# Optimization experiments

Measured on AMD Instinct MI355X. Metric: run time of the kernel, lower is better.

## Reference

```python
import jax, jax.numpy as jnp
import numpy as np

N_NODES = 50000
N_EDGES = 1_600_000
IN_DIM = 256
OUT_DIM = 128
NEG_SLOPE = 0.01  # F.leaky_relu default


def setup_inputs() -> dict:
    key = jax.random.key(0)
    k1, k2, k3, k4, k5 = jax.random.split(key, 5)
    x = jax.random.normal(k1, (N_NODES, IN_DIM), dtype=jnp.float32)
    # glorot_init: uniform in [-r, r], r = sqrt(6/(in+out))
    r = np.sqrt(6.0 / (IN_DIM + OUT_DIM)).astype(np.float32)
    weight = jax.random.uniform(k2, (IN_DIM, OUT_DIM), dtype=jnp.float32, minval=-r, maxval=r)
    adj_rows = jax.random.randint(k3, (N_EDGES,), 0, N_NODES, dtype=jnp.int64 if jax.config.jax_enable_x64 else jnp.int32)
    adj_cols = jax.random.randint(k4, (N_EDGES,), 0, N_NODES, dtype=jnp.int64 if jax.config.jax_enable_x64 else jnp.int32)
    adj_vals = jax.random.uniform(k5, (N_EDGES,), dtype=jnp.float32)
    return {"x": x, "weight": weight, "adj_vals": adj_vals,
            "adj_rows": adj_rows, "adj_cols": adj_cols}


def reference(x, weight, adj_vals, adj_rows, adj_cols):
    # h = X @ W : [N, OUT_DIM]
    h = x @ weight
    # sparse adj @ h via edge-list SpMM: out[r] += v * h[c]
    msgs = adj_vals[:, None] * h[adj_cols]            # [E, OUT_DIM]
    agg = jax.ops.segment_sum(msgs, adj_rows, num_segments=N_NODES)
    # leaky_relu epilogue
    return jnp.where(agg >= 0, agg, NEG_SLOPE * agg)
```

## Files before the change

### kernel.cpp

```cpp
#include <hip/hip_runtime.h>
#include <hip/hip_fp16.h>

#define N_NODES 50000
#define N_EDGES 1600000
#define IN_DIM 256
#define OUT_DIM 128
#define NEG_SLOPE 0.01f

#define BIN_SH    7
#define BIN_ROWS  128
#define NBIN      ((N_NODES + BIN_ROWS - 1) / BIN_ROWS)
#define CAPB      4864
#define ROWOFF_N  (NBIN * BIN_ROWS + 1)

#define GBLK_ROWS 32
#define NGBLK     ((N_NODES + GBLK_ROWS - 1) / GBLK_ROWS)

#define HIST_BLOCKS 512
#define CONVW_BLOCKS 16
#define EPB_H (N_EDGES / HIST_BLOCKS)
#define SCAT_BLOCKS 512
#define EPB_S (N_EDGES / SCAT_BLOCKS)
#define SCAT_ITERS ((EPB_S + 511) / 512)

typedef _Float16 f16x8 __attribute__((ext_vector_type(8)));
typedef float    f32x4 __attribute__((ext_vector_type(4)));
typedef float    f32x8 __attribute__((ext_vector_type(8)));

__device__ __forceinline__ float lrelu(float v) {
    return v >= 0.f ? v : NEG_SLOPE * v;
}

#define BM 128
#define GEMM_BLOCKS ((N_NODES + BM - 1) / BM)

#define CVT16(lo, hi) do { \
    lo[0]=(_Float16)xr[0].x; lo[1]=(_Float16)xr[0].y; lo[2]=(_Float16)xr[0].z; lo[3]=(_Float16)xr[0].w; \
    lo[4]=(_Float16)xr[1].x; lo[5]=(_Float16)xr[1].y; lo[6]=(_Float16)xr[1].z; lo[7]=(_Float16)xr[1].w; \
    hi[0]=(_Float16)xr[2].x; hi[1]=(_Float16)xr[2].y; hi[2]=(_Float16)xr[2].z; hi[3]=(_Float16)xr[2].w; \
    hi[4]=(_Float16)xr[3].x; hi[5]=(_Float16)xr[3].y; hi[6]=(_Float16)xr[3].z; hi[7]=(_Float16)xr[3].w; \
} while (0)

__global__ __launch_bounds__(256, 2) void gemm_xw_mfma(const float* __restrict__ x,
                                                       const __half* __restrict__ wtl,
                                                       __half* __restrict__ h) {
    __shared__ f16x8 wt8[32 * 128];
    __shared__ f16x8 xs8[2][4][BM];

    const int t    = threadIdx.x;
    const int lane = t & 63;
    const int wv   = t >> 6;
    const int row0 = blockIdx.x * BM;

    {
        const int4* src = (const int4*)wtl;
        int4* dst = (int4*)wt8;
#pragma unroll
        for (int i = 0; i < 16; ++i) dst[i * 256 + t] = src[i * 256 + t];
    }

    const int srow = t >> 1;
    const int skh  = t & 1;
    const int grow = row0 + srow;
    const bool rv  = grow < N_NODES;
    const float* xp = x + (size_t)(rv ? grow : 0) * IN_DIM + skh * 16;

    float4 xr[4];
#pragma unroll
    for (int i = 0; i < 4; ++i)
        xr[i] = rv ? ((const float4*)xp)[i] : make_float4(0.f, 0.f, 0.f, 0.f);
    {
        f16x8 lo, hi;
        CVT16(lo, hi);
        xs8[0][skh * 2 + 0][srow] = lo;
        xs8[0][skh * 2 + 1][srow] = hi;
    }
    __syncthreads();

    f32x4 acc[2][8];
#pragma unroll
    for (int mf = 0; mf < 2; ++mf)
#pragma unroll
        for (int nf = 0; nf < 8; ++nf) acc[mf][nf] = (f32x4){0.f, 0.f, 0.f, 0.f};

    const int kg  = lane >> 4;
    const int l15 = lane & 15;
    const int mb  = (wv << 5) + l15;

#pragma unroll
    for (int ks = 0; ks < 8; ++ks) {
        const int cur = ks & 1;
        if (ks < 7) {
#pragma unroll
            for (int i = 0; i < 4; ++i)
                xr[i] = rv ? ((const float4*)(xp + (ks + 1) * 32))[i]
                           : make_float4(0.f, 0.f, 0.f, 0.f);
        }
        const f16x8 b0 = xs8[cur][kg][mb];
        const f16x8 b1 = xs8[cur][kg][mb + 16];
#pragma unroll
        for (int nf = 0; nf < 8; ++nf) {
            const f16x8 a = wt8[(((ks << 2) | kg) << 7) + (nf << 4) + l15];
            acc[0][nf] = __builtin_amdgcn_mfma_f32_16x16x32_f16(a, b0, acc[0][nf], 0, 0, 0);
            acc[1][nf] = __builtin_amdgcn_mfma_f32_16x16x32_f16(a, b1, acc[1][nf], 0, 0, 0);
        }
        if (ks < 7) {
            f16x8 lo, hi;
            CVT16(lo, hi);
            xs8[cur ^ 1][skh * 2 + 0][srow] = lo;
            xs8[cur ^ 1][skh * 2 + 1][srow] = hi;
            __syncthreads();
        }
    }

    const int rg = lane >> 4;
#pragma unroll
    for (int mf = 0; mf < 2; ++mf) {
        const int m = row0 + (wv << 5) + (mf << 4) + l15;
        if (m < N_NODES) {
            __half* hp = h + (size_t)m * OUT_DIM + (rg << 2);
#pragma unroll
            for (int nf = 0; nf < 8; ++nf) {
                union { ushort4 u; __half f[4]; } o;
                o.f[0] = __float2half(acc[mf][nf][0]);
                o.f[1] = __float2half(acc[mf][nf][1]);
                o.f[2] = __float2half(acc[mf][nf][2]);
                o.f[3] = __float2half(acc[mf][nf][3]);
                *(ushort4*)(hp + (nf << 4)) = o.u;
            }
        }
    }
}

__global__ __launch_bounds__(256) void bucket_hist(const int* __restrict__ rows,
                                                   int* __restrict__ counts,
                                                   const float* __restrict__ w,
                                                   __half* __restrict__ wtl) {
    if (blockIdx.x >= HIST_BLOCKS) {
        const int e0 = ((blockIdx.x - HIST_BLOCKS) * 256 + threadIdx.x) * 8;
        const int k  = e0 >> 7;
        const int n0 = e0 & 127;
        const float4 a = *(const float4*)(w + e0);
        const float4 b = *(const float4*)(w + e0 + 4);
        __half* dst = wtl + ((size_t)((k >> 3) * 128 + n0)) * 8 + (k & 7);
        dst[0]  = __float2half(a.x);
        dst[8]  = __float2half(a.y);
        dst[16] = __float2half(a.z);
        dst[24] = __float2half(a.w);
        dst[32] = __float2half(b.x);
        dst[40] = __float2half(b.y);
        dst[48] = __float2half(b.z);
        dst[56] = __float2half(b.w);
        return;
    }

    __shared__ int lhist[NBIN];
    const int t = threadIdx.x;
    const int ebase = blockIdx.x * EPB_H;

    for (int b = t; b < NBIN; b += 256) lhist[b] = 0;
    __syncthreads();

    for (int k = 0; k < EPB_H; k += 256) {
        if (k + t < EPB_H) atomicAdd(&lhist[rows[ebase + k + t] >> BIN_SH], 1);
    }
    __syncthreads();

    for (int b = t; b < NBIN; b += 256) {
        const int c = lhist[b];
        if (c > 0) atomicAdd(&counts[b], c);
    }
}

__global__ __launch_bounds__(512) void scatter_bins(const int* __restrict__ rows,
                                                    const int* __restrict__ cols,
                                                    const float* __restrict__ vals,
                                                    const int* __restrict__ counts,
                                                    int* __restrict__ cursor,
                                                    int2* __restrict__ ebuf) {
    __shared__ int sb[512];
    __shared__ int lbase[NBIN];
    const int t = threadIdx.x;
    const int ebase = blockIdx.x * EPB_S;

    sb[t] = (t < NBIN) ? counts[t] : 0;
    const int myc = sb[t];
    __syncthreads();
    for (int off = 1; off < 512; off <<= 1) {
        const int u = (t >= off) ? sb[t - off] : 0;
        __syncthreads();
        sb[t] += u;
        __syncthreads();
    }
    if (t < NBIN) lbase[t] = sb[t] - myc;
    __syncthreads();
    if (t < NBIN) sb[t] = 0;
    __syncthreads();

    int myr[SCAT_ITERS];
#pragma unroll
    for (int k = 0; k < SCAT_ITERS; ++k) {
        const int i = k * 512 + t;
        myr[k] = -1;
        if (i < EPB_S) {
            const int r = rows[ebase + i];
            myr[k] = r;
            atomicAdd(&sb[r >> BIN_SH], 1);
        }
    }
    __syncthreads();

    if (t < NBIN) {
        const int c = sb[t];
        sb[t] = (c > 0) ? (lbase[t] + atomicAdd(&cursor[t], c)) : 0;
    }
    __syncthreads();

#pragma unroll
    for (int k = 0; k < SCAT_ITERS; ++k) {
        const int i = k * 512 + t;
        if (i < EPB_S) {
            const int e = ebase + i;
            const int r = myr[k];
            const int pos = atomicAdd(&sb[r >> BIN_SH], 1);
            ebuf[pos] = make_int2(cols[e] | ((r & (BIN_ROWS - 1)) << 16), __float_as_int(vals[e]));
        }
    }
}

__global__ __launch_bounds__(512) void sort_bins(const int* __restrict__ counts,
                                                 int2* __restrict__ ebuf,
                                                 int* __restrict__ rowoff,
                                                 int* __restrict__ ovf) {
    __shared__ int2 srec[CAPB];
    __shared__ int sb[512];
    __shared__ int hist[BIN_ROWS];
    __shared__ int pfx[BIN_ROWS];
    __shared__ int s_base, s_cnt;

    const int t   = threadIdx.x;
    const int bin = blockIdx.x;

    sb[t] = (t < NBIN) ? counts[t] : 0;
    const int myc = sb[t];
    __syncthreads();
    for (int off = 1; off < 512; off <<= 1) {
        const int u = (t >= off) ? sb[t - off] : 0;
        __syncthreads();
        sb[t] += u;
        __syncthreads();
    }
    if (t == bin) { s_base = sb[t] - myc; s_cnt = myc; }
    if (t < BIN_ROWS) hist[t] = 0;
    __syncthreads();
    const int base = s_base;
    const int cnt  = s_cnt;

    if (cnt <= CAPB) {
        for (int i = t; i < cnt; i += 512) {
            const int2 r = ebuf[base + i];
            srec[i] = r;
            atomicAdd(&hist[(r.x >> 16) & (BIN_ROWS - 1)], 1);
        }
        __syncthreads();

        if (t < BIN_ROWS) pfx[t] = hist[t];
        __syncthreads();
        for (int off = 1; off < BIN_ROWS; off <<= 1) {
            const int u = (t >= off && t < BIN_ROWS) ? pfx[t - off] : 0;
            __syncthreads();
            if (t < BIN_ROWS) pfx[t] += u;
            __syncthreads();
        }
        if (t < BIN_ROWS) {
            const int excl = pfx[t] - hist[t];
            rowoff[(bin << BIN_SH) + t] = base + excl;
            if (t == BIN_ROWS - 1) rowoff[(bin << BIN_SH) + BIN_ROWS] = base + cnt;
            hist[t] = excl;
        }
        __syncthreads();

        for (int i = t; i < cnt; i += 512) {
            const int2 r = srec[i];
            const int pos = base + atomicAdd(&hist[(r.x >> 16) & (BIN_ROWS - 1)], 1);
            ebuf[pos] = r;
        }
    } else {
        if (t == 0) ovf[bin] = 1;
        for (int i = t; i < cnt; i += 512)
            atomicAdd(&hist[(ebuf[base + i].x >> 16) & (BIN_ROWS - 1)], 1);
        __syncthreads();
        if (t < BIN_ROWS) pfx[t] = hist[t];
        __syncthreads();
        for (int off = 1; off < BIN_ROWS; off <<= 1) {
            const int u = (t >= off && t < BIN_ROWS) ? pfx[t - off] : 0;
            __syncthreads();
            if (t < BIN_ROWS) pfx[t] += u;
            __syncthreads();
        }
        if (t < BIN_ROWS) {
            rowoff[(bin << BIN_SH) + t] = base + (pfx[t] - hist[t]);
            if (t == BIN_ROWS - 1) rowoff[(bin << BIN_SH) + BIN_ROWS] = base + cnt;
        }
    }
}

__global__ __launch_bounds__(256) void gather_rows(const __half* __restrict__ h,
                                                   const int* __restrict__ rowoff,
                                                   const int2* __restrict__ ebuf,
                                                   const int* __restrict__ ovf,
                                                   float* __restrict__ out) {
    const int t    = threadIdx.x;
    const int w    = t >> 6;
    const int lane = t & 63;
    const int grp  = lane >> 4;
    const int gl   = lane & 15;
    const int bkt  = blockIdx.x;
    const int bin  = bkt >> 2;
    const int rbase = bkt * GBLK_ROWS + w * 8;

    if (ovf[bin]) {
        const int bb = rowoff[bin << BIN_SH];
        const int be = rowoff[(bin << BIN_SH) + BIN_ROWS];
        for (int rr = 0; rr < 8; ++rr) {
            const int row = rbase + rr;
            float2 acc = make_float2(0.f, 0.f);
            for (int e = bb; e < be; ++e) {
                const int2 rec = ebuf[e];
                if (((rec.x >> 16) & (BIN_ROWS - 1)) == (row & (BIN_ROWS - 1))) {
                    const float2 m = __half22float2(((const __half2*)(h + (size_t)(rec.x & 0xFFFF) * OUT_DIM))[lane]);
                    const float v = __int_as_float(rec.y);
                    acc.x += v * m.x; acc.y += v * m.y;
                }
            }
            if (row < N_NODES) {
                acc.x = lrelu(acc.x); acc.y = lrelu(acc.y);
                ((float2*)(out + (size_t)row * OUT_DIM))[lane] = acc;
            }
        }
        return;
    }

    for (int p = 0; p < 4; ++p) {
        const int r0 = rbase + 2 * p;
        const int r1 = r0 + 1;
        const int b0 = rowoff[r0], e0 = rowoff[r0 + 1];
        const int b1 = rowoff[r1], e1 = rowoff[r1 + 1];
        const int n0 = e0 - b0, n1 = e1 - b1;
        const int nmax = n0 > n1 ? n0 : n1;
        const int iters = (nmax + 3) >> 2;

        f32x8 a0 = (f32x8){0.f,0.f,0.f,0.f,0.f,0.f,0.f,0.f};
        f32x8 a1 = (f32x8){0.f,0.f,0.f,0.f,0.f,0.f,0.f,0.f};

        for (int it = 0; it < iters; ++it) {
            const int i0 = b0 + (it << 2) + grp;
            const int i1 = b1 + (it << 2) + grp;
            const bool v0i = i0 < e0;
            const bool v1i = i1 < e1;
            const int2 rA = ebuf[v0i ? i0 : 0];
            const int2 rB = ebuf[v1i ? i1 : 0];
            const float vA = v0i ? __int_as_float(rA.y) : 0.f;
            const float vB = v1i ? __int_as_float(rB.y) : 0.f;
            const f16x8 hA = *(const f16x8*)(h + (size_t)(rA.x & 0xFFFF) * OUT_DIM + (gl << 3));
            const f16x8 hB = *(const f16x8*)(h + (size_t)(rB.x & 0xFFFF) * OUT_DIM + (gl << 3));
#pragma unroll
            for (int j = 0; j < 8; ++j) {
                a0[j] += vA * (float)hA[j];
                a1[j] += vB * (float)hB[j];
            }
        }

#pragma unroll
        for (int j = 0; j < 8; ++j) {
            float x0 = a0[j], x1 = a1[j];
            x0 += __shfl_xor(x0, 16); x0 += __shfl_xor(x0, 32);
            x1 += __shfl_xor(x1, 16); x1 += __shfl_xor(x1, 32);
            a0[j] = x0; a1[j] = x1;
        }

        const int row = (grp & 2) ? r1 : r0;
        float q[4];
#pragma unroll
        for (int k = 0; k < 4; ++k) {
            const float lo = (grp & 2) ? a1[k]     : a0[k];
            const float hi = (grp & 2) ? a1[k + 4] : a0[k + 4];
            q[k] = lrelu((grp & 1) ? hi : lo);
        }
        if (row < N_NODES) {
            float4 o = make_float4(q[0], q[1], q[2], q[3]);
            *(float4*)(out + (size_t)row * OUT_DIM + (gl << 3) + ((grp & 1) << 2)) = o;
        }
    }
}

extern "C" void kernel_launch(void* const* d_in, const int* in_sizes, int n_in,
                              void* d_out, int out_size, void* d_ws, size_t ws_size,
                              hipStream_t stream) {
    const float* x    = (const float*)d_in[0];
    const float* w    = (const float*)d_in[1];
    const float* vals = (const float*)d_in[2];
    const int*   rows = (const int*)d_in[3];
    const int*   cols = (const int*)d_in[4];
    float* out = (float*)d_out;

    char* ws = (char*)d_ws;
    size_t off = 0;
    auto alloc = [&](size_t bytes) {
        void* p = ws + off;
        off = (off + bytes + 255) & ~(size_t)255;
        return p;
    };
    __half* h      = (__half*)alloc((size_t)N_NODES * OUT_DIM * sizeof(__half));
    int2*  ebuf    = (int2*) alloc((size_t)N_EDGES * sizeof(int2));
    __half* wtl    = (__half*)alloc((size_t)IN_DIM * OUT_DIM * sizeof(__half));
    int*   rowoff  = (int*)  alloc((size_t)ROWOFF_N * sizeof(int));
    int*   meta    = (int*)  alloc((size_t)(3 * NBIN) * sizeof(int));
    int*   counts  = meta;
    int*   cursor  = meta + NBIN;
    int*   ovfl    = meta + 2 * NBIN;

    hipMemsetAsync(meta, 0, (size_t)(3 * NBIN) * sizeof(int), stream);

    bucket_hist<<<HIST_BLOCKS + CONVW_BLOCKS, 256, 0, stream>>>(rows, counts, w, wtl);
    gemm_xw_mfma<<<GEMM_BLOCKS, 256, 0, stream>>>(x, wtl, h);
    scatter_bins<<<SCAT_BLOCKS, 512, 0, stream>>>(rows, cols, vals, counts, cursor, ebuf);
    sort_bins<<<NBIN, 512, 0, stream>>>(counts, ebuf, rowoff, ovfl);
    gather_rows<<<NGBLK, 256, 0, stream>>>(h, rowoff, ebuf, ovfl, out);
}
```

Baseline: 238.6 us.

## Fuse per-bin sort with row gather, keeping sorted edges in LDS

Merges the sort_bins and gather_rows kernels into a single sort_gather kernel. Each block sorts its bin's edges straight into shared memory and then runs the SpMM gather for its 128 rows using LDS row offsets. This removes the write-back of sorted edges to global memory, the rowoff and overflow arrays, and one kernel launch. In exchange the gather now runs with only 391 blocks of 512 threads and heavy LDS use, so fewer rows are in flight per CU during the latency-bound h gathers.

```diff
diff --git a/kernel.cpp b/kernel.cpp
--- a/kernel.cpp
+++ b/kernel.cpp
@@ -11,10 +11,6 @@
 #define BIN_ROWS  128
 #define NBIN      ((N_NODES + BIN_ROWS - 1) / BIN_ROWS)
 #define CAPB      4864
-#define ROWOFF_N  (NBIN * BIN_ROWS + 1)
-
-#define GBLK_ROWS 32
-#define NGBLK     ((N_NODES + GBLK_ROWS - 1) / GBLK_ROWS)
 
 #define HIST_BLOCKS 512
 #define CONVW_BLOCKS 16
@@ -228,18 +224,19 @@
     }
 }
 
-__global__ __launch_bounds__(512) void sort_bins(const int* __restrict__ counts,
-                                                 int2* __restrict__ ebuf,
-                                                 int* __restrict__ rowoff,
-                                                 int* __restrict__ ovf) {
+__global__ __launch_bounds__(512) void sort_gather(const int* __restrict__ counts,
+                                                   const int2* __restrict__ ebuf,
+                                                   const __half* __restrict__ h,
+                                                   float* __restrict__ out) {
     __shared__ int2 srec[CAPB];
-    __shared__ int sb[512];
-    __shared__ int hist[BIN_ROWS];
-    __shared__ int pfx[BIN_ROWS];
-    __shared__ int s_base, s_cnt;
+    __shared__ int  hist[BIN_ROWS];
+    __shared__ int  pfx[BIN_ROWS];
+    __shared__ int  rowoff_l[BIN_ROWS + 1];
+    __shared__ int  s_base, s_cnt;
 
     const int t   = threadIdx.x;
     const int bin = blockIdx.x;
+    int* sb = (int*)srec;
 
     sb[t] = (t < NBIN) ? counts[t] : 0;
     const int myc = sb[t];
@@ -256,12 +253,12 @@
     const int base = s_base;
     const int cnt  = s_cnt;
 
+    const int wv   = t >> 6;
+    const int lane = t & 63;
+
     if (cnt <= CAPB) {
-        for (int i = t; i < cnt; i += 512) {
-            const int2 r = ebuf[base + i];
-            srec[i] = r;
-            atomicAdd(&hist[(r.x >> 16) & (BIN_ROWS - 1)], 1);
-        }
+        for (int i = t; i < cnt; i += 512)
+            atomicAdd(&hist[(ebuf[base + i].x >> 16) & (BIN_ROWS - 1)], 1);
         __syncthreads();
 
         if (t < BIN_ROWS) pfx[t] = hist[t];
@@ -274,122 +271,90 @@
         }
         if (t < BIN_ROWS) {
             const int excl = pfx[t] - hist[t];
-            rowoff[(bin << BIN_SH) + t] = base + excl;
-            if (t == BIN_ROWS - 1) rowoff[(bin << BIN_SH) + BIN_ROWS] = base + cnt;
+            rowoff_l[t] = excl;
+            if (t == BIN_ROWS - 1) rowoff_l[BIN_ROWS] = cnt;
             hist[t] = excl;
         }
         __syncthreads();
 
         for (int i = t; i < cnt; i += 512) {
-            const int2 r = srec[i];
-            const int pos = base + atomicAdd(&hist[(r.x >> 16) & (BIN_ROWS - 1)], 1);
-            ebuf[pos] = r;
+            const int2 r = ebuf[base + i];
+            const int pos = atomicAdd(&hist[(r.x >> 16) & (BIN_ROWS - 1)], 1);
+            srec[pos] = r;
+        }
+        __syncthreads();
+
+        const int grp = lane >> 4;
+        const int gl  = lane & 15;
+        for (int rp = 0; rp < 8; ++rp) {
+            const int lr0 = (wv << 4) + 2 * rp;
+            const int lr1 = lr0 + 1;
+            const int b0 = rowoff_l[lr0], e0 = rowoff_l[lr0 + 1];
+            const int b1 = rowoff_l[lr1], e1 = rowoff_l[lr1 + 1];
+            const int n0 = e0 - b0, n1 = e1 - b1;
+            const int nmax = n0 > n1 ? n0 : n1;
+            const int iters = (nmax + 3) >> 2;
+
+            f32x8 a0 = (f32x8){0.f,0.f,0.f,0.f,0.f,0.f,0.f,0.f};
+            f32x8 a1 = (f32x8){0.f,0.f,0.f,0.f,0.f,0.f,0.f,0.f};
+
+            for (int it = 0; it < iters; ++it) {
+                const int i0 = b0 + (it << 2) + grp;
+                const int i1 = b1 + (it << 2) + grp;
+                const bool v0i = i0 < e0;
+                const bool v1i = i1 < e1;
+                const int2 rA = srec[v0i ? i0 : 0];
+                const int2 rB = srec[v1i ? i1 : 0];
+                const float vA = v0i ? __int_as_float(rA.y) : 0.f;
+                const float vB = v1i ? __int_as_float(rB.y) : 0.f;
+                const f16x8 hA = *(const f16x8*)(h + (size_t)(rA.x & 0xFFFF) * OUT_DIM + (gl << 3));
+                const f16x8 hB = *(const f16x8*)(h + (size_t)(rB.x & 0xFFFF) * OUT_DIM + (gl << 3));
+#pragma unroll
+                for (int j = 0; j < 8; ++j) {
+                    a0[j] += vA * (float)hA[j];
+                    a1[j] += vB * (float)hB[j];
+                }
+            }
+
+#pragma unroll
+            for (int j = 0; j < 8; ++j) {
+                float x0 = a0[j], x1 = a1[j];
+                x0 += __shfl_xor(x0, 16); x0 += __shfl_xor(x0, 32);
+                x1 += __shfl_xor(x1, 16); x1 += __shfl_xor(x1, 32);
+                a0[j] = x0; a1[j] = x1;
+            }
+
+            const int lrow = (grp & 2) ? lr1 : lr0;
+            const int grow = (bin << BIN_SH) + lrow;
+            float q[4];
+#pragma unroll
+            for (int k = 0; k < 4; ++k) {
+                const float lo = (grp & 2) ? a1[k]     : a0[k];
+                const float hi = (grp & 2) ? a1[k + 4] : a0[k + 4];
+                q[k] = lrelu((grp & 1) ? hi : lo);
+            }
+            if (grow < N_NODES) {
+                float4 o = make_float4(q[0], q[1], q[2], q[3]);
+                *(float4*)(out + (size_t)grow * OUT_DIM + (gl << 3) + ((grp & 1) << 2)) = o;
+            }
         }
     } else {
-        if (t == 0) ovf[bin] = 1;
-        for (int i = t; i < cnt; i += 512)
-            atomicAdd(&hist[(ebuf[base + i].x >> 16) & (BIN_ROWS - 1)], 1);
-        __syncthreads();
-        if (t < BIN_ROWS) pfx[t] = hist[t];
-        __syncthreads();
-        for (int off = 1; off < BIN_ROWS; off <<= 1) {
-            const int u = (t >= off && t < BIN_ROWS) ? pfx[t - off] : 0;
-            __syncthreads();
-            if (t < BIN_ROWS) pfx[t] += u;
-            __syncthreads();
-        }
-        if (t < BIN_ROWS) {
-            rowoff[(bin << BIN_SH) + t] = base + (pfx[t] - hist[t]);
-            if (t == BIN_ROWS - 1) rowoff[(bin << BIN_SH) + BIN_ROWS] = base + cnt;
-        }
-    }
-}
-
-__global__ __launch_bounds__(256) void gather_rows(const __half* __restrict__ h,
-                                                   const int* __restrict__ rowoff,
-                                                   const int2* __restrict__ ebuf,
-                                                   const int* __restrict__ ovf,
-                                                   float* __restrict__ out) {
-    const int t    = threadIdx.x;
-    const int w    = t >> 6;
-    const int lane = t & 63;
-    const int grp  = lane >> 4;
-    const int gl   = lane & 15;
-    const int bkt  = blockIdx.x;
-    const int bin  = bkt >> 2;
-    const int rbase = bkt * GBLK_ROWS + w * 8;
-
-    if (ovf[bin]) {
-        const int bb = rowoff[bin << BIN_SH];
-        const int be = rowoff[(bin << BIN_SH) + BIN_ROWS];
-        for (int rr = 0; rr < 8; ++rr) {
-            const int row = rbase + rr;
+        for (int rr = 0; rr < 16; ++rr) {
+            const int lr = (wv << 4) + rr;
             float2 acc = make_float2(0.f, 0.f);
-            for (int e = bb; e < be; ++e) {
-                const int2 rec = ebuf[e];
-                if (((rec.x >> 16) & (BIN_ROWS - 1)) == (row & (BIN_ROWS - 1))) {
+            for (int e = 0; e < cnt; ++e) {
+                const int2 rec = ebuf[base + e];
+                if (((rec.x >> 16) & (BIN_ROWS - 1)) == lr) {
                     const float2 m = __half22float2(((const __half2*)(h + (size_t)(rec.x & 0xFFFF) * OUT_DIM))[lane]);
                     const float v = __int_as_float(rec.y);
                     acc.x += v * m.x; acc.y += v * m.y;
                 }
             }
-            if (row < N_NODES) {
+            const int grow = (bin << BIN_SH) + lr;
+            if (grow < N_NODES) {
                 acc.x = lrelu(acc.x); acc.y = lrelu(acc.y);
-                ((float2*)(out + (size_t)row * OUT_DIM))[lane] = acc;
-            }
-        }
-        return;
-    }
-
-    for (int p = 0; p < 4; ++p) {
-        const int r0 = rbase + 2 * p;
-        const int r1 = r0 + 1;
-        const int b0 = rowoff[r0], e0 = rowoff[r0 + 1];
-        const int b1 = rowoff[r1], e1 = rowoff[r1 + 1];
-        const int n0 = e0 - b0, n1 = e1 - b1;
-        const int nmax = n0 > n1 ? n0 : n1;
-        const int iters = (nmax + 3) >> 2;
-
-        f32x8 a0 = (f32x8){0.f,0.f,0.f,0.f,0.f,0.f,0.f,0.f};
-        f32x8 a1 = (f32x8){0.f,0.f,0.f,0.f,0.f,0.f,0.f,0.f};
-
-        for (int it = 0; it < iters; ++it) {
-            const int i0 = b0 + (it << 2) + grp;
-            const int i1 = b1 + (it << 2) + grp;
-            const bool v0i = i0 < e0;
-            const bool v1i = i1 < e1;
-            const int2 rA = ebuf[v0i ? i0 : 0];
-            const int2 rB = ebuf[v1i ? i1 : 0];
-            const float vA = v0i ? __int_as_float(rA.y) : 0.f;
-            const float vB = v1i ? __int_as_float(rB.y) : 0.f;
-            const f16x8 hA = *(const f16x8*)(h + (size_t)(rA.x & 0xFFFF) * OUT_DIM + (gl << 3));
-            const f16x8 hB = *(const f16x8*)(h + (size_t)(rB.x & 0xFFFF) * OUT_DIM + (gl << 3));
-#pragma unroll
-            for (int j = 0; j < 8; ++j) {
-                a0[j] += vA * (float)hA[j];
-                a1[j] += vB * (float)hB[j];
-            }
-        }
-
-#pragma unroll
-        for (int j = 0; j < 8; ++j) {
-            float x0 = a0[j], x1 = a1[j];
-            x0 += __shfl_xor(x0, 16); x0 += __shfl_xor(x0, 32);
-            x1 += __shfl_xor(x1, 16); x1 += __shfl_xor(x1, 32);
-            a0[j] = x0; a1[j] = x1;
-        }
-
-        const int row = (grp & 2) ? r1 : r0;
-        float q[4];
-#pragma unroll
-        for (int k = 0; k < 4; ++k) {
-            const float lo = (grp & 2) ? a1[k]     : a0[k];
-            const float hi = (grp & 2) ? a1[k + 4] : a0[k + 4];
-            q[k] = lrelu((grp & 1) ? hi : lo);
-        }
-        if (row < N_NODES) {
-            float4 o = make_float4(q[0], q[1], q[2], q[3]);
-            *(float4*)(out + (size_t)row * OUT_DIM + (gl << 3) + ((grp & 1) << 2)) = o;
+                ((float2*)(out + (size_t)grow * OUT_DIM))[lane] = acc;
+            }
         }
     }
 }
@@ -414,17 +379,14 @@
     __half* h      = (__half*)alloc((size_t)N_NODES * OUT_DIM * sizeof(__half));
     int2*  ebuf    = (int2*) alloc((size_t)N_EDGES * sizeof(int2));
     __half* wtl    = (__half*)alloc((size_t)IN_DIM * OUT_DIM * sizeof(__half));
-    int*   rowoff  = (int*)  alloc((size_t)ROWOFF_N * sizeof(int));
-    int*   meta    = (int*)  alloc((size_t)(3 * NBIN) * sizeof(int));
+    int*   meta    = (int*)  alloc((size_t)(2 * NBIN) * sizeof(int));
     int*   counts  = meta;
     int*   cursor  = meta + NBIN;
-    int*   ovfl    = meta + 2 * NBIN;
-
-    hipMemsetAsync(meta, 0, (size_t)(3 * NBIN) * sizeof(int), stream);
+
+    hipMemsetAsync(meta, 0, (size_t)(2 * NBIN) * sizeof(int), stream);
 
     bucket_hist<<<HIST_BLOCKS + CONVW_BLOCKS, 256, 0, stream>>>(rows, counts, w, wtl);
     gemm_xw_mfma<<<GEMM_BLOCKS, 256, 0, stream>>>(x, wtl, h);
     scatter_bins<<<SCAT_BLOCKS, 512, 0, stream>>>(rows, cols, vals, counts, cursor, ebuf);
-    sort_bins<<<NBIN, 512, 0, stream>>>(counts, ebuf, rowoff, ovfl);
-    gather_rows<<<NGBLK, 256, 0, stream>>>(h, rowoff, ebuf, ovfl, out);
-}
+    sort_gather<<<NBIN, 512, 0, stream>>>(counts, ebuf, h, out);
+}
```

Result: faster. 228.3 us (-4.3%).
